# Optimization experiments

Measured on AMD Instinct MI355X. Metric: run time of the kernel, lower is better.

The kernel has to match this reference:

```python
import jax, jax.numpy as jnp
import numpy as np

N = 50000      # nodes
E = 800000     # edges
F_IN = 11      # node feature dim (from docstring)
HID = 128      # hidden_channels
NC = 16        # num_classes
G = 64         # number of graphs in the batch
NEG_SLOPE = 0.2


def gat_layer(h_in, src, dst, W, a_src, a_dst, b, n_nodes):
    """Single-head GATConv with self-loops (PyG defaults, edge_attr unused)."""
    h = h_in @ W                                   # [N, C]
    alpha_s = h @ a_src                            # [N]
    alpha_d = h @ a_dst                            # [N]
    e = jax.nn.leaky_relu(alpha_s[src] + alpha_d[dst], NEG_SLOPE)  # [E']
    # segment softmax over incoming edges of each dst node
    m = jax.ops.segment_max(e, dst, num_segments=n_nodes)
    ex = jnp.exp(e - m[dst])
    den = jax.ops.segment_sum(ex, dst, num_segments=n_nodes)
    alpha = ex / den[dst]                          # [E']
    out = jax.ops.segment_sum(alpha[:, None] * h[src], dst, num_segments=n_nodes)
    return out + b


def setup_inputs() -> dict:
    key = jax.random.key(0)
    ks = jax.random.split(key, 16)
    glorot = lambda k, fi, fo: jax.random.normal(k, (fi, fo), jnp.float32) * np.float32(1.0 / np.sqrt(fi))
    inp = {
        "x": jax.random.normal(ks[0], (N, F_IN), jnp.float32),
        "edge_index": jax.random.randint(ks[1], (2, E), 0, N, dtype=jnp.int32),
        "edge_attr": jax.random.normal(ks[2], (E, 17), jnp.float32),
        "batch": jnp.sort(jax.random.randint(ks[3], (N,), 0, G, dtype=jnp.int32)),
        "W1": glorot(ks[4], F_IN, HID), "as1": jax.random.normal(ks[5], (HID,)) * 0.1,
        "ad1": jax.random.normal(ks[6], (HID,)) * 0.1, "b1": jnp.zeros((HID,), jnp.float32),
        "W2": glorot(ks[7], HID, HID), "as2": jax.random.normal(ks[8], (HID,)) * 0.1,
        "ad2": jax.random.normal(ks[9], (HID,)) * 0.1, "b2": jnp.zeros((HID,), jnp.float32),
        "W3": glorot(ks[10], HID, NC), "as3": jax.random.normal(ks[11], (NC,)) * 0.1,
        "ad3": jax.random.normal(ks[12], (NC,)) * 0.1, "b3": jnp.zeros((NC,), jnp.float32),
    }
    return inp


def reference(x, edge_index, edge_attr, batch,
              W1, as1, ad1, b1, W2, as2, ad2, b2, W3, as3, ad3, b3):
    n = x.shape[0]
    loop = jnp.arange(n, dtype=edge_index.dtype)
    src = jnp.concatenate([edge_index[0], loop])   # add self-loops
    dst = jnp.concatenate([edge_index[1], loop])

    h = jax.nn.relu(gat_layer(x, src, dst, W1, as1, ad1, b1, n))
    h = jax.nn.relu(gat_layer(h, src, dst, W2, as2, ad2, b2, n))
    h = jax.nn.relu(gat_layer(h, src, dst, W3, as3, ad3, b3, n))

    # global mean pool over graphs
    sums = jax.ops.segment_sum(h, batch, num_segments=G)              # [G, NC]
    cnts = jax.ops.segment_sum(jnp.ones((n,), h.dtype), batch, num_segments=G)
    pooled = sums / jnp.maximum(cnts, 1.0)[:, None]
    # dropout is identity in eval mode
    return jax.nn.sigmoid(pooled)
```

## Files before the change

### kernel.cpp

```cpp
#include <hip/hip_runtime.h>
#include <hip/hip_bf16.h>
#include <hip/hip_fp16.h>
#include <math.h>

#define N_NODES 50000
#define N_EDGES 800000
#define F_IN    11
#define HID     128
#define NC      16
#define NG      64
#define E_TOT   (N_EDGES + N_NODES)
#define NBLK_POOL ((N_NODES + 255) / 256)
#define NEG_SLOPE 0.2f

#define NB   ((N_NODES + 63) >> 6)
#define BCAP 4096

typedef _Float16 half_t;
typedef __attribute__((ext_vector_type(4))) _Float16 half4;

__device__ __forceinline__ float leaky(float x) { return x >= 0.f ? x : NEG_SLOPE * x; }


__global__ void zero_nb_kernel(int* __restrict__ gcount) {
    int i = threadIdx.x;
    if (i < NB) gcount[i] = 0;
}

__global__ __launch_bounds__(256) void bucket_hist_kernel(const int* __restrict__ ei,
                                                          int* __restrict__ gcount) {
    __shared__ int cnt[NB];
    int tid = threadIdx.x;
    for (int i = tid; i < NB; i += 256) cnt[i] = 0;
    __syncthreads();
    int e0 = blockIdx.x * 4096 + tid;
#pragma unroll
    for (int k = 0; k < 16; ++k) {
        int e = e0 + k * 256;
        if (e < N_EDGES) atomicAdd(&cnt[ei[N_EDGES + e] >> 6], 1);
    }
    __syncthreads();
    for (int i = tid; i < NB; i += 256)
        if (cnt[i]) atomicAdd(&gcount[i], cnt[i]);
}

__global__ void scanB_kernel(const int* __restrict__ gcount, int* __restrict__ bOff,
                             int* __restrict__ gcur) {
    __shared__ int ls[1024];
    int tid = threadIdx.x;
    int v = 0;
    if (tid < NB) {
        int sl = N_NODES - (tid << 6);
        sl = sl > 64 ? 64 : sl;
        v = gcount[tid] + sl;
    }
    ls[tid] = v;
    __syncthreads();
    for (int ofs = 1; ofs < 1024; ofs <<= 1) {
        int x = (tid >= ofs) ? ls[tid - ofs] : 0;
        __syncthreads();
        ls[tid] += x;
        __syncthreads();
    }
    int excl = (tid > 0) ? ls[tid - 1] : 0;
    if (tid < NB) { bOff[tid] = excl; gcur[tid] = excl; }
    if (tid == 0) bOff[NB] = E_TOT;
}

__global__ __launch_bounds__(256) void bucket_scatter_kernel(const int* __restrict__ ei,
                                                             int* __restrict__ gcur,
                                                             uint2* __restrict__ pairs) {
    __shared__ int cnt[NB];
    __shared__ int base[NB];
    int tid = threadIdx.x;
    for (int i = tid; i < NB; i += 256) cnt[i] = 0;
    __syncthreads();
    int s[16], d[16];
    int e0 = blockIdx.x * 4096 + tid;
#pragma unroll
    for (int k = 0; k < 16; ++k) {
        int e = e0 + k * 256;
        if (e < N_EDGES) { s[k] = ei[e]; d[k] = ei[N_EDGES + e]; }
        else if (e < E_TOT) { s[k] = d[k] = e - N_EDGES; }
        else d[k] = -1;
        if (d[k] >= 0) atomicAdd(&cnt[d[k] >> 6], 1);
    }
    __syncthreads();
    for (int i = tid; i < NB; i += 256)
        base[i] = cnt[i] ? atomicAdd(&gcur[i], cnt[i]) : 0;
    __syncthreads();
    for (int i = tid; i < NB; i += 256) cnt[i] = 0;
    __syncthreads();
#pragma unroll
    for (int k = 0; k < 16; ++k) {
        if (d[k] >= 0) {
            int b = d[k] >> 6;
            int r = atomicAdd(&cnt[b], 1);
            pairs[base[b] + r] = make_uint2((unsigned)s[k], (unsigned)d[k]);
        }
    }
}

__global__ __launch_bounds__(256) void csr_finalize_kernel(const uint2* __restrict__ pairs,
                                                           const int* __restrict__ bOff,
                                                           int* __restrict__ off,
                                                           int* __restrict__ csr) {
    __shared__ uint2 lp[BCAP];
    __shared__ int deg[64], offs[65], cnt[64];
    int b = blockIdx.x, tid = threadIdx.x;
    int d0 = b << 6;
    int nd = N_NODES - d0; nd = nd > 64 ? 64 : nd;
    int lo = bOff[b], hi = bOff[b + 1], n = hi - lo;
    if (tid < 64) { deg[tid] = 0; cnt[tid] = 0; }
    __syncthreads();
    bool staged = (n <= BCAP);
    for (int i = tid; i < n; i += 256) {
        uint2 p = pairs[lo + i];
        if (staged) lp[i] = p;
        atomicAdd(&deg[(int)p.y - d0], 1);
    }
    __syncthreads();
    if (tid == 0) {
        int a = 0;
#pragma unroll
        for (int i = 0; i < 64; ++i) { offs[i] = a; a += deg[i]; }
        offs[64] = a;
    }
    __syncthreads();
    if (tid < nd) off[d0 + tid] = lo + offs[tid];
    if (b == (int)gridDim.x - 1 && tid == 0) off[N_NODES] = E_TOT;
    for (int i = tid; i < n; i += 256) {
        uint2 p = staged ? lp[i] : pairs[lo + i];
        int ld = (int)p.y - d0;
        int r = atomicAdd(&cnt[ld], 1);
        csr[lo + offs[ld] + r] = (int)p.x;
    }
}


__global__ void gemm1_kernel(const float* __restrict__ x, const float* __restrict__ W,
                             float* __restrict__ h, half_t* __restrict__ h16) {
    __shared__ float xr[F_IN];
    int row = blockIdx.x;
    int t = threadIdx.x;
    if (t < F_IN) xr[t] = x[row * F_IN + t];
    __syncthreads();
    float acc = 0.f;
#pragma unroll
    for (int k = 0; k < F_IN; ++k) acc = fmaf(xr[k], W[k * HID + t], acc);
    h[(size_t)row * HID + t] = acc;
    h16[(size_t)row * HID + t] = (half_t)acc;
}

__global__ __launch_bounds__(256) void gemm2_kernel(const float* __restrict__ A,
                                                    const float* __restrict__ W,
                                                    float* __restrict__ outp,
                                                    half_t* __restrict__ h16) {
    __shared__ float hs[16][HID];
    int tid = threadIdx.x;
    int row0 = blockIdx.x * 16;
    for (int i = tid; i < 16 * HID; i += 256) {
        int r = i >> 7, c = i & 127;
        int gr = row0 + r;
        hs[r][c] = (gr < N_NODES) ? A[(size_t)gr * HID + c] : 0.f;
    }
    __syncthreads();
    int col = tid & 127, rg = tid >> 7;
    float acc[8] = {0.f, 0.f, 0.f, 0.f, 0.f, 0.f, 0.f, 0.f};
    for (int k4 = 0; k4 < HID / 4; ++k4) {
        float4 hv[8];
#pragma unroll
        for (int r = 0; r < 8; ++r)
            hv[r] = *(const float4*)&hs[rg * 8 + r][k4 * 4];
#pragma unroll
        for (int kk = 0; kk < 4; ++kk) {
            float w = W[(k4 * 4 + kk) * HID + col];
#pragma unroll
            for (int r = 0; r < 8; ++r)
                acc[r] = fmaf(((const float*)&hv[r])[kk], w, acc[r]);
        }
    }
#pragma unroll
    for (int r = 0; r < 8; ++r) {
        int gr = row0 + rg * 8 + r;
        if (gr < N_NODES) {
            outp[(size_t)gr * HID + col] = acc[r];
            h16[(size_t)gr * HID + col] = (half_t)acc[r];
        }
    }
}

__global__ __launch_bounds__(256) void gemm3_kernel(const float* __restrict__ A,
                                                    const float* __restrict__ W,
                                                    float* __restrict__ outp) {
    __shared__ float hs[16][HID + 1];
    int tid = threadIdx.x;
    int row0 = blockIdx.x * 16;
    for (int i = tid; i < 16 * HID; i += 256) {
        int r = i >> 7, c = i & 127;
        int gr = row0 + r;
        hs[r][c] = (gr < N_NODES) ? A[(size_t)gr * HID + c] : 0.f;
    }
    __syncthreads();
    int col = tid & 15, r = tid >> 4;
    float acc = 0.f;
#pragma unroll 4
    for (int k = 0; k < HID; ++k) acc = fmaf(hs[r][k], W[k * NC + col], acc);
    int gr = row0 + r;
    if (gr < N_NODES) outp[(size_t)gr * NC + col] = acc;
}


template <int C>
__global__ void alpha_kernel(const float* __restrict__ h, const float* __restrict__ a_s,
                             const float* __restrict__ a_d, float* __restrict__ asv,
                             float* __restrict__ adv) {
    int lane = threadIdx.x & 63;
    int n = (blockIdx.x * blockDim.x + threadIdx.x) >> 6;
    if (n >= N_NODES) return;
    float ps = 0.f, pd = 0.f;
#pragma unroll
    for (int c = lane; c < C; c += 64) {
        float v = h[(size_t)n * C + c];
        ps = fmaf(v, a_s[c], ps);
        pd = fmaf(v, a_d[c], pd);
    }
#pragma unroll
    for (int k = 32; k; k >>= 1) {
        ps += __shfl_xor(ps, k);
        pd += __shfl_xor(pd, k);
    }
    if (lane == 0) { asv[n] = ps; adv[n] = pd; }
}


__global__ __launch_bounds__(256) void agg128_kernel(
    const half_t* __restrict__ h16, const int* __restrict__ off, const int* __restrict__ csr,
    const float* __restrict__ asv, const float* __restrict__ adv,
    const float* __restrict__ bias, float* __restrict__ outp) {
    int lane = threadIdx.x & 63;
    int n = (blockIdx.x * blockDim.x + threadIdx.x) >> 6;
    if (n >= N_NODES) return;
    int o0 = off[n], o1 = off[n + 1];
    float ad_n = adv[n];
    int half = lane >> 5;
    int qc = lane & 31;
    const half4* hp = (const half4*)h16;
    float m = -INFINITY, den = 0.f;
    float4 acc = make_float4(0.f, 0.f, 0.f, 0.f);
    for (int base = o0; base < o1; base += 64) {
        int j = base + lane;
        bool valid = j < o1;
        int s = valid ? csr[j] : 0;
        float e = valid ? leaky(asv[s] + ad_n) : -INFINITY;
        float cm = e;
#pragma unroll
        for (int k = 32; k; k >>= 1) cm = fmaxf(cm, __shfl_xor(cm, k));
        float nm = fmaxf(m, cm);
        float rs = __expf(m - nm);
        den *= rs; acc.x *= rs; acc.y *= rs; acc.z *= rs; acc.w *= rs;
        float w = valid ? __expf(e - nm) : 0.f;
        float ws = w;
#pragma unroll
        for (int k = 32; k; k >>= 1) ws += __shfl_xor(ws, k);
        den += ws;
        m = nm;
        int cnt = min(64, o1 - base);
        int t = 0;
        for (; t + 8 <= cnt; t += 8) {
            int e0 = t + half, e1 = t + 2 + half, e2 = t + 4 + half, e3 = t + 6 + half;
            int s0 = __shfl(s, e0), s1 = __shfl(s, e1), s2 = __shfl(s, e2), s3 = __shfl(s, e3);
            float w0 = __shfl(w, e0), w1 = __shfl(w, e1), w2 = __shfl(w, e2), w3 = __shfl(w, e3);
            half4 v0 = hp[(size_t)s0 * 32 + qc];
            half4 v1 = hp[(size_t)s1 * 32 + qc];
            half4 v2 = hp[(size_t)s2 * 32 + qc];
            half4 v3 = hp[(size_t)s3 * 32 + qc];
            acc.x = fmaf(w0, (float)v0.x, acc.x); acc.y = fmaf(w0, (float)v0.y, acc.y);
            acc.z = fmaf(w0, (float)v0.z, acc.z); acc.w = fmaf(w0, (float)v0.w, acc.w);
            acc.x = fmaf(w1, (float)v1.x, acc.x); acc.y = fmaf(w1, (float)v1.y, acc.y);
            acc.z = fmaf(w1, (float)v1.z, acc.z); acc.w = fmaf(w1, (float)v1.w, acc.w);
            acc.x = fmaf(w2, (float)v2.x, acc.x); acc.y = fmaf(w2, (float)v2.y, acc.y);
            acc.z = fmaf(w2, (float)v2.z, acc.z); acc.w = fmaf(w2, (float)v2.w, acc.w);
            acc.x = fmaf(w3, (float)v3.x, acc.x); acc.y = fmaf(w3, (float)v3.y, acc.y);
            acc.z = fmaf(w3, (float)v3.z, acc.z); acc.w = fmaf(w3, (float)v3.w, acc.w);
        }
        for (; t + 2 <= cnt; t += 2) {
            int e0 = t + half;
            int s0 = __shfl(s, e0);
            float w0 = __shfl(w, e0);
            half4 v0 = hp[(size_t)s0 * 32 + qc];
            acc.x = fmaf(w0, (float)v0.x, acc.x); acc.y = fmaf(w0, (float)v0.y, acc.y);
            acc.z = fmaf(w0, (float)v0.z, acc.z); acc.w = fmaf(w0, (float)v0.w, acc.w);
        }
        if (t < cnt) {
            int s0 = __shfl(s, t);
            float w0 = __shfl(w, t);
            if (half == 0) {
                half4 v0 = hp[(size_t)s0 * 32 + qc];
                acc.x = fmaf(w0, (float)v0.x, acc.x); acc.y = fmaf(w0, (float)v0.y, acc.y);
                acc.z = fmaf(w0, (float)v0.z, acc.z); acc.w = fmaf(w0, (float)v0.w, acc.w);
            }
        }
    }
    acc.x += __shfl_xor(acc.x, 32); acc.y += __shfl_xor(acc.y, 32);
    acc.z += __shfl_xor(acc.z, 32); acc.w += __shfl_xor(acc.w, 32);
    if (half == 0) {
        float inv = 1.f / den;
        float4 bv = ((const float4*)bias)[qc];
        float4 o;
        o.x = fmaxf(fmaf(acc.x, inv, bv.x), 0.f);
        o.y = fmaxf(fmaf(acc.y, inv, bv.y), 0.f);
        o.z = fmaxf(fmaf(acc.z, inv, bv.z), 0.f);
        o.w = fmaxf(fmaf(acc.w, inv, bv.w), 0.f);
        ((float4*)outp)[(size_t)n * 32 + qc] = o;
    }
}

__global__ __launch_bounds__(256) void agg16_kernel(
    const float* __restrict__ h, const int* __restrict__ off, const int* __restrict__ csr,
    const float* __restrict__ asv, const float* __restrict__ adv,
    const float* __restrict__ bias, float* __restrict__ outp) {
    int lane = threadIdx.x & 63;
    int n = (blockIdx.x * blockDim.x + threadIdx.x) >> 6;
    if (n >= N_NODES) return;
    int o0 = off[n], o1 = off[n + 1];
    float ad_n = adv[n];
    int g = lane >> 3, pr = lane & 7;
    const float2* hp = (const float2*)h;
    float m = -INFINITY, den = 0.f;
    float ax = 0.f, ay = 0.f;
    for (int base = o0; base < o1; base += 64) {
        int j = base + lane;
        bool valid = j < o1;
        int s = valid ? csr[j] : 0;
        float e = valid ? leaky(asv[s] + ad_n) : -INFINITY;
        float cm = e;
#pragma unroll
        for (int k = 32; k; k >>= 1) cm = fmaxf(cm, __shfl_xor(cm, k));
        float nm = fmaxf(m, cm);
        float rs = __expf(m - nm);
        den *= rs; ax *= rs; ay *= rs;
        float w = valid ? __expf(e - nm) : 0.f;
        float ws = w;
#pragma unroll
        for (int k = 32; k; k >>= 1) ws += __shfl_xor(ws, k);
        den += ws;
        m = nm;
        int cnt = min(64, o1 - base);
        for (int t = g; t < cnt; t += 8) {
            int st = __shfl(s, t);
            float wt = __shfl(w, t);
            float2 v = hp[(size_t)st * 8 + pr];
            ax = fmaf(wt, v.x, ax); ay = fmaf(wt, v.y, ay);
        }
    }
    ax += __shfl_xor(ax, 8);  ay += __shfl_xor(ay, 8);
    ax += __shfl_xor(ax, 16); ay += __shfl_xor(ay, 16);
    ax += __shfl_xor(ax, 32); ay += __shfl_xor(ay, 32);
    if (g == 0) {
        float inv = 1.f / den;
        float vx = fmaxf(fmaf(ax, inv, bias[pr * 2]), 0.f);
        float vy = fmaxf(fmaf(ay, inv, bias[pr * 2 + 1]), 0.f);
        ((float2*)outp)[(size_t)n * 8 + pr] = make_float2(vx, vy);
    }
}


__global__ void pool_partial_kernel(const float* __restrict__ h3, const int* __restrict__ batch,
                                    float* __restrict__ part) {
    __shared__ float sp[NG * 17];
    int tid = threadIdx.x;
    for (int i = tid; i < NG * 17; i += 256) sp[i] = 0.f;
    __syncthreads();
    int n = blockIdx.x * 256 + tid;
    if (n < N_NODES) {
        int g = batch[n];
        const float4* hv = (const float4*)(h3 + (size_t)n * NC);
#pragma unroll
        for (int j = 0; j < 4; ++j) {
            float4 v = hv[j];
            atomicAdd(&sp[g * 17 + j * 4 + 0], v.x);
            atomicAdd(&sp[g * 17 + j * 4 + 1], v.y);
            atomicAdd(&sp[g * 17 + j * 4 + 2], v.z);
            atomicAdd(&sp[g * 17 + j * 4 + 3], v.w);
        }
        atomicAdd(&sp[g * 17 + 16], 1.f);
    }
    __syncthreads();
    for (int i = tid; i < NG * 17; i += 256) part[(size_t)blockIdx.x * (NG * 17) + i] = sp[i];
}

__global__ void pool_final_kernel(const float* __restrict__ part, float* __restrict__ outp) {
    int tid = threadIdx.x;
    int g = tid >> 4, c = tid & 15;
    float sum = 0.f, cnt = 0.f;
    for (int b = 0; b < NBLK_POOL; ++b) {
        sum += part[(size_t)b * (NG * 17) + g * 17 + c];
        cnt += part[(size_t)b * (NG * 17) + g * 17 + 16];
    }
    float v = sum / fmaxf(cnt, 1.f);
    outp[g * NC + c] = 1.f / (1.f + __expf(-v));
}


extern "C" void kernel_launch(void* const* d_in, const int* in_sizes, int n_in,
                              void* d_out, int out_size, void* d_ws, size_t ws_size,
                              hipStream_t stream) {
    const float* x   = (const float*)d_in[0];
    const int*   ei  = (const int*)d_in[1];
    const int*   bat = (const int*)d_in[3];
    const float* W1  = (const float*)d_in[4];
    const float* as1 = (const float*)d_in[5];
    const float* ad1 = (const float*)d_in[6];
    const float* b1  = (const float*)d_in[7];
    const float* W2  = (const float*)d_in[8];
    const float* as2 = (const float*)d_in[9];
    const float* ad2 = (const float*)d_in[10];
    const float* b2  = (const float*)d_in[11];
    const float* W3  = (const float*)d_in[12];
    const float* as3 = (const float*)d_in[13];
    const float* ad3 = (const float*)d_in[14];
    const float* b3  = (const float*)d_in[15];
    float* outp = (float*)d_out;

    char* p = (char*)d_ws;
    auto carve = [&](size_t bytes) {
        char* r = p;
        p += (bytes + 255) & ~(size_t)255;
        return r;
    };
    int*    off    = (int*)carve((size_t)(N_NODES + 1) * 4);
    int*    csr    = (int*)carve((size_t)E_TOT * 4);
    int*    gcount = (int*)carve((size_t)NB * 4);
    int*    bOff   = (int*)carve((size_t)(NB + 1) * 4);
    int*    gcur   = (int*)carve((size_t)NB * 4);
    float*  hA     = (float*)carve((size_t)N_NODES * HID * 4);
    float*  hB     = (float*)carve((size_t)N_NODES * HID * 4);
    half_t* h16    = (half_t*)carve((size_t)N_NODES * HID * 2);
    float*  asv    = (float*)carve((size_t)N_NODES * 4);
    float*  adv    = (float*)carve((size_t)N_NODES * 4);
    float*  part   = (float*)carve((size_t)NBLK_POOL * NG * 17 * 4);
    uint2* pairs  = (uint2*)hB;

    zero_nb_kernel<<<1, 1024, 0, stream>>>(gcount);
    bucket_hist_kernel<<<(N_EDGES + 4095) / 4096, 256, 0, stream>>>(ei, gcount);
    scanB_kernel<<<1, 1024, 0, stream>>>(gcount, bOff, gcur);
    bucket_scatter_kernel<<<(E_TOT + 4095) / 4096, 256, 0, stream>>>(ei, gcur, pairs);
    csr_finalize_kernel<<<NB, 256, 0, stream>>>(pairs, bOff, off, csr);

    gemm1_kernel<<<N_NODES, 128, 0, stream>>>(x, W1, hA, h16);
    alpha_kernel<HID><<<(N_NODES + 3) / 4, 256, 0, stream>>>(hA, as1, ad1, asv, adv);
    agg128_kernel<<<(N_NODES + 3) / 4, 256, 0, stream>>>(h16, off, csr, asv, adv, b1, hB);

    gemm2_kernel<<<(N_NODES + 15) / 16, 256, 0, stream>>>(hB, W2, hA, h16);
    alpha_kernel<HID><<<(N_NODES + 3) / 4, 256, 0, stream>>>(hA, as2, ad2, asv, adv);
    agg128_kernel<<<(N_NODES + 3) / 4, 256, 0, stream>>>(h16, off, csr, asv, adv, b2, hB);

    gemm3_kernel<<<(N_NODES + 15) / 16, 256, 0, stream>>>(hB, W3, hA);
    alpha_kernel<NC><<<(N_NODES + 3) / 4, 256, 0, stream>>>(hA, as3, ad3, asv, adv);
    agg16_kernel<<<(N_NODES + 3) / 4, 256, 0, stream>>>(hA, off, csr, asv, adv, b3, hB);

    pool_partial_kernel<<<NBLK_POOL, 256, 0, stream>>>(hB, bat, part);
    pool_final_kernel<<<1, 1024, 0, stream>>>(part, outp);
}
```

Before: 393.6 us.

## Fuse attention-logit dot products into GEMMs, use MFMA fp16 for layer-2 GEMM

Removes the three separate alpha kernels by computing the source and destination attention logits inside each GEMM epilogue with wave shuffles. The hidden 128x128 GEMM now runs on fp16 MFMA instructions using a pre-transposed fp16 copy of W2. Intermediate activations are stored only in fp16, which halves the bytes written by the aggregation kernels and read by the next GEMM. This trades fp32 precision in the intermediate features and logits for fewer launches and less memory traffic.

```diff
diff --git a/kernel.cpp b/kernel.cpp
--- a/kernel.cpp
+++ b/kernel.cpp
@@ -18,6 +18,8 @@
 
 typedef _Float16 half_t;
 typedef __attribute__((ext_vector_type(4))) _Float16 half4;
+typedef __attribute__((ext_vector_type(8))) _Float16 half8;
+typedef __attribute__((ext_vector_type(4))) float f32x4;
 
 __device__ __forceinline__ float leaky(float x) { return x >= 0.f ? x : NEG_SLOPE * x; }
 
@@ -138,9 +140,21 @@
 }
 
 
+__global__ void prep_w2t_kernel(const float* __restrict__ W2, half_t* __restrict__ W2T) {
+    int id = blockIdx.x * 256 + threadIdx.x;
+    if (id < HID * HID) {
+        int col = id >> 7, k = id & 127;
+        W2T[id] = (half_t)W2[k * HID + col];
+    }
+}
+
+
 __global__ void gemm1_kernel(const float* __restrict__ x, const float* __restrict__ W,
-                             float* __restrict__ h, half_t* __restrict__ h16) {
+                             const float* __restrict__ a_s, const float* __restrict__ a_d,
+                             half_t* __restrict__ h16,
+                             float* __restrict__ asv, float* __restrict__ adv) {
     __shared__ float xr[F_IN];
+    __shared__ float red[4];
     int row = blockIdx.x;
     int t = threadIdx.x;
     if (t < F_IN) xr[t] = x[row * F_IN + t];
@@ -148,58 +162,79 @@
     float acc = 0.f;
 #pragma unroll
     for (int k = 0; k < F_IN; ++k) acc = fmaf(xr[k], W[k * HID + t], acc);
-    h[(size_t)row * HID + t] = acc;
     h16[(size_t)row * HID + t] = (half_t)acc;
-}
-
-__global__ __launch_bounds__(256) void gemm2_kernel(const float* __restrict__ A,
+    float ps = acc * a_s[t], pd = acc * a_d[t];
+#pragma unroll
+    for (int m = 32; m; m >>= 1) { ps += __shfl_xor(ps, m); pd += __shfl_xor(pd, m); }
+    int lane = t & 63, wid = t >> 6;
+    if (lane == 0) { red[wid * 2] = ps; red[wid * 2 + 1] = pd; }
+    __syncthreads();
+    if (t == 0) { asv[row] = red[0] + red[2]; adv[row] = red[1] + red[3]; }
+}
+
+
+__global__ __launch_bounds__(256) void gemm2_mfma_kernel(
+    const half_t* __restrict__ A, const half_t* __restrict__ W2T,
+    const float* __restrict__ a_s, const float* __restrict__ a_d,
+    half_t* __restrict__ outp, float* __restrict__ asv, float* __restrict__ adv) {
+    int wid = threadIdx.x >> 6;
+    int lane = threadIdx.x & 63;
+    int row0 = blockIdx.x * 64 + wid * 16;
+    int rl = lane & 15;
+    int kg = lane >> 4;
+    int arow = row0 + rl;
+    if (arow >= N_NODES) arow = N_NODES - 1;
+    const half8* Ap = (const half8*)(A + (size_t)arow * HID);
+    half8 afrag[4];
+#pragma unroll
+    for (int kk = 0; kk < 4; ++kk) afrag[kk] = Ap[kk * 4 + kg];
+    float ps[4] = {0.f, 0.f, 0.f, 0.f}, pd[4] = {0.f, 0.f, 0.f, 0.f};
+#pragma unroll
+    for (int ct = 0; ct < 8; ++ct) {
+        f32x4 acc = {0.f, 0.f, 0.f, 0.f};
+        const half8* Bp = (const half8*)(W2T + (size_t)(ct * 16 + rl) * HID);
+#pragma unroll
+        for (int kk = 0; kk < 4; ++kk)
+            acc = __builtin_amdgcn_mfma_f32_16x16x32_f16(afrag[kk], Bp[kk * 4 + kg], acc, 0, 0, 0);
+        int col = ct * 16 + rl;
+        float as_c = a_s[col], ad_c = a_d[col];
+#pragma unroll
+        for (int i = 0; i < 4; ++i) {
+            int r = row0 + kg * 4 + i;
+            ps[i] = fmaf(acc[i], as_c, ps[i]);
+            pd[i] = fmaf(acc[i], ad_c, pd[i]);
+            if (r < N_NODES) outp[(size_t)r * HID + col] = (half_t)acc[i];
+        }
+    }
+#pragma unroll
+    for (int m = 1; m <= 8; m <<= 1) {
+#pragma unroll
+        for (int i = 0; i < 4; ++i) { ps[i] += __shfl_xor(ps[i], m); pd[i] += __shfl_xor(pd[i], m); }
+    }
+    if (rl == 0) {
+#pragma unroll
+        for (int i = 0; i < 4; ++i) {
+            int r = row0 + kg * 4 + i;
+            if (r < N_NODES) { asv[r] = ps[i]; adv[r] = pd[i]; }
+        }
+    }
+}
+
+
+__global__ __launch_bounds__(256) void gemm3_kernel(const half_t* __restrict__ A16,
                                                     const float* __restrict__ W,
+                                                    const float* __restrict__ a_s,
+                                                    const float* __restrict__ a_d,
                                                     float* __restrict__ outp,
-                                                    half_t* __restrict__ h16) {
-    __shared__ float hs[16][HID];
+                                                    float* __restrict__ asv,
+                                                    float* __restrict__ adv) {
+    __shared__ float hs[16][HID + 1];
     int tid = threadIdx.x;
     int row0 = blockIdx.x * 16;
     for (int i = tid; i < 16 * HID; i += 256) {
         int r = i >> 7, c = i & 127;
         int gr = row0 + r;
-        hs[r][c] = (gr < N_NODES) ? A[(size_t)gr * HID + c] : 0.f;
-    }
-    __syncthreads();
-    int col = tid & 127, rg = tid >> 7;
-    float acc[8] = {0.f, 0.f, 0.f, 0.f, 0.f, 0.f, 0.f, 0.f};
-    for (int k4 = 0; k4 < HID / 4; ++k4) {
-        float4 hv[8];
-#pragma unroll
-        for (int r = 0; r < 8; ++r)
-            hv[r] = *(const float4*)&hs[rg * 8 + r][k4 * 4];
-#pragma unroll
-        for (int kk = 0; kk < 4; ++kk) {
-            float w = W[(k4 * 4 + kk) * HID + col];
-#pragma unroll
-            for (int r = 0; r < 8; ++r)
-                acc[r] = fmaf(((const float*)&hv[r])[kk], w, acc[r]);
-        }
-    }
-#pragma unroll
-    for (int r = 0; r < 8; ++r) {
-        int gr = row0 + rg * 8 + r;
-        if (gr < N_NODES) {
-            outp[(size_t)gr * HID + col] = acc[r];
-            h16[(size_t)gr * HID + col] = (half_t)acc[r];
-        }
-    }
-}
-
-__global__ __launch_bounds__(256) void gemm3_kernel(const float* __restrict__ A,
-                                                    const float* __restrict__ W,
-                                                    float* __restrict__ outp) {
-    __shared__ float hs[16][HID + 1];
-    int tid = threadIdx.x;
-    int row0 = blockIdx.x * 16;
-    for (int i = tid; i < 16 * HID; i += 256) {
-        int r = i >> 7, c = i & 127;
-        int gr = row0 + r;
-        hs[r][c] = (gr < N_NODES) ? A[(size_t)gr * HID + c] : 0.f;
+        hs[r][c] = (gr < N_NODES) ? (float)A16[(size_t)gr * HID + c] : 0.f;
     }
     __syncthreads();
     int col = tid & 15, r = tid >> 4;
@@ -207,37 +242,20 @@
 #pragma unroll 4
     for (int k = 0; k < HID; ++k) acc = fmaf(hs[r][k], W[k * NC + col], acc);
     int gr = row0 + r;
-    if (gr < N_NODES) outp[(size_t)gr * NC + col] = acc;
-}
-
-
-template <int C>
-__global__ void alpha_kernel(const float* __restrict__ h, const float* __restrict__ a_s,
-                             const float* __restrict__ a_d, float* __restrict__ asv,
-                             float* __restrict__ adv) {
-    int lane = threadIdx.x & 63;
-    int n = (blockIdx.x * blockDim.x + threadIdx.x) >> 6;
-    if (n >= N_NODES) return;
-    float ps = 0.f, pd = 0.f;
-#pragma unroll
-    for (int c = lane; c < C; c += 64) {
-        float v = h[(size_t)n * C + c];
-        ps = fmaf(v, a_s[c], ps);
-        pd = fmaf(v, a_d[c], pd);
-    }
-#pragma unroll
-    for (int k = 32; k; k >>= 1) {
-        ps += __shfl_xor(ps, k);
-        pd += __shfl_xor(pd, k);
-    }
-    if (lane == 0) { asv[n] = ps; adv[n] = pd; }
+    float ps = acc * a_s[col], pd = acc * a_d[col];
+#pragma unroll
+    for (int m = 1; m <= 8; m <<= 1) { ps += __shfl_xor(ps, m); pd += __shfl_xor(pd, m); }
+    if (gr < N_NODES) {
+        outp[(size_t)gr * NC + col] = acc;
+        if (col == 0) { asv[gr] = ps; adv[gr] = pd; }
+    }
 }
 
 
 __global__ __launch_bounds__(256) void agg128_kernel(
     const half_t* __restrict__ h16, const int* __restrict__ off, const int* __restrict__ csr,
     const float* __restrict__ asv, const float* __restrict__ adv,
-    const float* __restrict__ bias, float* __restrict__ outp) {
+    const float* __restrict__ bias, half_t* __restrict__ outp) {
     int lane = threadIdx.x & 63;
     int n = (blockIdx.x * blockDim.x + threadIdx.x) >> 6;
     if (n >= N_NODES) return;
@@ -307,12 +325,12 @@
     if (half == 0) {
         float inv = 1.f / den;
         float4 bv = ((const float4*)bias)[qc];
-        float4 o;
-        o.x = fmaxf(fmaf(acc.x, inv, bv.x), 0.f);
-        o.y = fmaxf(fmaf(acc.y, inv, bv.y), 0.f);
-        o.z = fmaxf(fmaf(acc.z, inv, bv.z), 0.f);
-        o.w = fmaxf(fmaf(acc.w, inv, bv.w), 0.f);
-        ((float4*)outp)[(size_t)n * 32 + qc] = o;
+        half4 o;
+        o.x = (half_t)fmaxf(fmaf(acc.x, inv, bv.x), 0.f);
+        o.y = (half_t)fmaxf(fmaf(acc.y, inv, bv.y), 0.f);
+        o.z = (half_t)fmaxf(fmaf(acc.z, inv, bv.z), 0.f);
+        o.w = (half_t)fmaxf(fmaf(acc.w, inv, bv.w), 0.f);
+        ((half4*)outp)[(size_t)n * 32 + qc] = o;
     }
 }
 
@@ -434,13 +452,15 @@
     int*    gcount = (int*)carve((size_t)NB * 4);
     int*    bOff   = (int*)carve((size_t)(NB + 1) * 4);
     int*    gcur   = (int*)carve((size_t)NB * 4);
-    float*  hA     = (float*)carve((size_t)N_NODES * HID * 4);
-    float*  hB     = (float*)carve((size_t)N_NODES * HID * 4);
+    uint2*  pairs  = (uint2*)carve((size_t)E_TOT * 8);
     half_t* h16    = (half_t*)carve((size_t)N_NODES * HID * 2);
+    half_t* o16    = (half_t*)carve((size_t)N_NODES * HID * 2);
+    half_t* W2T    = (half_t*)carve((size_t)HID * HID * 2);
+    float*  h3     = (float*)carve((size_t)N_NODES * NC * 4);
+    float*  o3     = (float*)carve((size_t)N_NODES * NC * 4);
     float*  asv    = (float*)carve((size_t)N_NODES * 4);
     float*  adv    = (float*)carve((size_t)N_NODES * 4);
     float*  part   = (float*)carve((size_t)NBLK_POOL * NG * 17 * 4);
-    uint2* pairs  = (uint2*)hB;
 
     zero_nb_kernel<<<1, 1024, 0, stream>>>(gcount);
     bucket_hist_kernel<<<(N_EDGES + 4095) / 4096, 256, 0, stream>>>(ei, gcount);
@@ -448,18 +468,17 @@
     bucket_scatter_kernel<<<(E_TOT + 4095) / 4096, 256, 0, stream>>>(ei, gcur, pairs);
     csr_finalize_kernel<<<NB, 256, 0, stream>>>(pairs, bOff, off, csr);
 
-    gemm1_kernel<<<N_NODES, 128, 0, stream>>>(x, W1, hA, h16);
-    alpha_kernel<HID><<<(N_NODES + 3) / 4, 256, 0, stream>>>(hA, as1, ad1, asv, adv);
-    agg128_kernel<<<(N_NODES + 3) / 4, 256, 0, stream>>>(h16, off, csr, asv, adv, b1, hB);
-
-    gemm2_kernel<<<(N_NODES + 15) / 16, 256, 0, stream>>>(hB, W2, hA, h16);
-    alpha_kernel<HID><<<(N_NODES + 3) / 4, 256, 0, stream>>>(hA, as2, ad2, asv, adv);
-    agg128_kernel<<<(N_NODES + 3) / 4, 256, 0, stream>>>(h16, off, csr, asv, adv, b2, hB);
-
-    gemm3_kernel<<<(N_NODES + 15) / 16, 256, 0, stream>>>(hB, W3, hA);
-    alpha_kernel<NC><<<(N_NODES + 3) / 4, 256, 0, stream>>>(hA, as3, ad3, asv, adv);
-    agg16_kernel<<<(N_NODES + 3) / 4, 256, 0, stream>>>(hA, off, csr, asv, adv, b3, hB);
-
-    pool_partial_kernel<<<NBLK_POOL, 256, 0, stream>>>(hB, bat, part);
+    prep_w2t_kernel<<<(HID * HID + 255) / 256, 256, 0, stream>>>(W2, W2T);
+
+    gemm1_kernel<<<N_NODES, 128, 0, stream>>>(x, W1, as1, ad1, h16, asv, adv);
+    agg128_kernel<<<(N_NODES + 3) / 4, 256, 0, stream>>>(h16, off, csr, asv, adv, b1, o16);
+
+    gemm2_mfma_kernel<<<(N_NODES + 63) / 64, 256, 0, stream>>>(o16, W2T, as2, ad2, h16, asv, adv);
+    agg128_kernel<<<(N_NODES + 3) / 4, 256, 0, stream>>>(h16, off, csr, asv, adv, b2, o16);
+
+    gemm3_kernel<<<(N_NODES + 15) / 16, 256, 0, stream>>>(o16, W3, as3, ad3, h3, asv, adv);
+    agg16_kernel<<<(N_NODES + 3) / 4, 256, 0, stream>>>(h3, off, csr, asv, adv, b3, o3);
+
+    pool_partial_kernel<<<NBLK_POOL, 256, 0, stream>>>(o3, bat, part);
     pool_final_kernel<<<1, 1024, 0, stream>>>(part, outp);
 }
```

Result: faster. 343.0 us (-12.9%).
